# Performance work log

Hardware: AMD Instinct MI355X
Metric: run time of the kernel (lower is better)

The kernel has to match this reference:

```python
import jax, jax.numpy as jnp
import numpy as np

NUM_TOKENS = 2048
NUM_EXPERTS = 8
TOPK = 2
INTERMEDIATE = 2048
HIDDEN = 1024


def setup_inputs() -> dict:
    key = jax.random.key(0)
    k1, k2, k3 = jax.random.split(key, 3)
    intermediate_states = jax.random.normal(k1, (NUM_TOKENS * TOPK, INTERMEDIATE), dtype=jnp.float32)
    # per-expert down-projection, scaled like a typical init
    w = jax.random.normal(k2, (NUM_EXPERTS, INTERMEDIATE, HIDDEN), dtype=jnp.float32) / np.float32(np.sqrt(INTERMEDIATE))
    router_logits = jax.random.normal(k3, (NUM_TOKENS, NUM_EXPERTS), dtype=jnp.float32)
    return {"intermediate_states": intermediate_states, "w": w, "router_logits": router_logits}


def reference(intermediate_states, w, router_logits):
    T, E = router_logits.shape
    K = TOPK
    H = w.shape[-1]
    # Routing: softmax over experts, then top-k weights/ids (precompute_ctx.full_topk_weight/full_topk_ids)
    probs = jax.nn.softmax(router_logits, axis=-1)          # [T, E]
    topk_w, topk_ids = jax.lax.top_k(probs, K)              # [T, K]
    # Grouped expert GEMM: each (token, k) row is multiplied by its expert's weight.
    # Compute against all experts once, then gather the routed expert per row.
    out_all = jnp.einsum('ri,eih->reh', intermediate_states, w)   # [T*K, E, H]
    flat_ids = topk_ids.reshape(-1)                               # [T*K]
    routed = jnp.take_along_axis(out_all, flat_ids[:, None, None], axis=1)[:, 0, :]  # [T*K, H]
    # topk-weighted reduction over the K expert outputs per token
    out = (routed.reshape(T, K, H) * topk_w[..., None]).sum(axis=1)  # [T, H]
    # reduce-scatter across tensor-parallel ranks: with world_size=1 this is identity
    return out
```

## Files before the change

### kernel.cpp

```cpp
#include <hip/hip_runtime.h>

#define T_TOKENS 2048
#define N_EXPERTS 8
#define ROWS (T_TOKENS * 2)
#define I_DIM 2048
#define H_DIM 1024

#define M_TILE 128
#define N_TILE 128
#define BK 64
#define KSPLIT 2
#define KCHUNK (I_DIM / KSPLIT)
#define NSTEP (KCHUNK / BK)

typedef __bf16 bf16x8 __attribute__((ext_vector_type(8)));
typedef float f32x4 __attribute__((ext_vector_type(4)));

__device__ inline void load_lds16(const void* g, void* l) {
    __builtin_amdgcn_global_load_lds(
        (const __attribute__((address_space(1))) void*)g,
        (__attribute__((address_space(3))) void*)l, 16, 0, 0);
}

__global__ __launch_bounds__(256) void prep_kernel(
    const float* __restrict__ w, const float* __restrict__ x,
    const float* __restrict__ logits,
    __bf16* __restrict__ wT, __bf16* __restrict__ xB,
    float* __restrict__ out, float* __restrict__ topk_w,
    int* __restrict__ cnt, int* __restrict__ rowlist) {
    const int b = blockIdx.x;
    const int t = threadIdx.x;
    if (b < 2048) {
        __shared__ float tile[128 * 65];
        const int e = b >> 8;
        const int k0 = ((b >> 4) & 15) * 128;
        const int n0 = (b & 15) * 64;
        const float* ws = w + (size_t)e * (I_DIM * H_DIM) + (size_t)k0 * H_DIM + n0;
#pragma unroll
        for (int i = 0; i < 8; ++i) {
            int flat = i * 256 + t;
            int k = flat >> 4, nq = (flat & 15) * 4;
            f32x4 v = *(const f32x4*)(ws + (size_t)k * H_DIM + nq);
            float* d = &tile[k * 65 + nq];
            d[0] = v.x; d[1] = v.y; d[2] = v.z; d[3] = v.w;
        }
        __syncthreads();
        __bf16* wd = wT + (size_t)e * (H_DIM * I_DIM) + (size_t)n0 * I_DIM + k0;
#pragma unroll
        for (int j = 0; j < 4; ++j) {
            int flat = j * 256 + t;
            int n = flat >> 4, kc = (flat & 15) * 8;
            bf16x8 o;
#pragma unroll
            for (int q = 0; q < 8; ++q) o[q] = (__bf16)tile[(kc + q) * 65 + n];
            *(bf16x8*)(wd + (size_t)n * I_DIM + kc) = o;
        }
    } else if (b < 4096) {
        size_t base = ((size_t)(b - 2048) * 256 + t) * 16;
        const f32x4* xs = (const f32x4*)(x + base);
        f32x4 v0 = xs[0], v1 = xs[1], v2 = xs[2], v3 = xs[3];
        bf16x8 o0 = { (__bf16)v0.x, (__bf16)v0.y, (__bf16)v0.z, (__bf16)v0.w,
                      (__bf16)v1.x, (__bf16)v1.y, (__bf16)v1.z, (__bf16)v1.w };
        bf16x8 o1 = { (__bf16)v2.x, (__bf16)v2.y, (__bf16)v2.z, (__bf16)v2.w,
                      (__bf16)v3.x, (__bf16)v3.y, (__bf16)v3.z, (__bf16)v3.w };
        *(bf16x8*)(xB + base) = o0;
        *(bf16x8*)(xB + base + 8) = o1;
    } else if (b < 5120) {
        size_t idx = (size_t)(b - 4096) * 256 + t;
        f32x4 z = (f32x4){0.f, 0.f, 0.f, 0.f};
        ((f32x4*)out)[2 * idx] = z;
        ((f32x4*)out)[2 * idx + 1] = z;
    } else {
        __shared__ int lcnt[N_EXPERTS];
        if (t < N_EXPERTS) lcnt[t] = 0;
        __syncthreads();
#pragma unroll
        for (int i = 0; i < 8; ++i) {
            int tok = i * 256 + t;
            float l[8];
#pragma unroll
            for (int e = 0; e < 8; ++e) l[e] = logits[tok * 8 + e];
            float mx = l[0];
#pragma unroll
            for (int e = 1; e < 8; ++e) mx = fmaxf(mx, l[e]);
            float s = 0.f;
#pragma unroll
            for (int e = 0; e < 8; ++e) { l[e] = expf(l[e] - mx); s += l[e]; }
            float inv = 1.f / s;
            float v0 = -1.f, v1 = -1.f; int i0 = 0, i1 = 0;
#pragma unroll
            for (int e = 0; e < 8; ++e) {
                float p = l[e] * inv;
                if (p > v0)      { v1 = v0; i1 = i0; v0 = p; i0 = e; }
                else if (p > v1) { v1 = p; i1 = e; }
            }
            topk_w[2 * tok]     = v0;
            topk_w[2 * tok + 1] = v1;
            int p0 = atomicAdd(&lcnt[i0], 1); rowlist[i0 * ROWS + p0] = 2 * tok;
            int p1 = atomicAdd(&lcnt[i1], 1); rowlist[i1 * ROWS + p1] = 2 * tok + 1;
        }
        __syncthreads();
        if (t < N_EXPERTS) cnt[t] = lcnt[t];
    }
}

__global__ __launch_bounds__(256, 2) void gemm_kernel(
    const __bf16* __restrict__ xB, const __bf16* __restrict__ wT,
    const int* __restrict__ cnt, const int* __restrict__ rowlist,
    const float* __restrict__ topk_w, float* __restrict__ out) {
    const int e = blockIdx.y;
    const int cnt_e = cnt[e];
    const int m0 = blockIdx.z * M_TILE;
    if (m0 >= cnt_e) return;
    const int ntile = blockIdx.x & 7;
    const int khalf = blockIdx.x >> 3;
    const int n0 = ntile * N_TILE;
    const int tid = threadIdx.x;
    const int lane = tid & 63;
    const int wave = tid >> 6;
    const int wm = wave & 1, wn = wave >> 1;

    __shared__ __bf16 As[2][M_TILE * BK];
    __shared__ __bf16 Bs[2][N_TILE * BK];

    const int* rl = rowlist + e * ROWS;

    const int lc = lane & 7;
    const int lr = lane >> 3;
    const int cg = lc ^ lr;

    const __bf16* asrc[4];
#pragma unroll
    for (int i = 0; i < 4; ++i) {
        int gm = m0 + 32 * wave + 8 * i + lr;
        if (gm >= cnt_e) gm = cnt_e - 1;
        asrc[i] = xB + (size_t)rl[gm] * I_DIM + khalf * KCHUNK + cg * 8;
    }
    const __bf16* wTe = wT + (size_t)e * (H_DIM * I_DIM);
    const __bf16* bsrc = wTe + (size_t)(n0 + 32 * wave + lr) * I_DIM
                             + khalf * KCHUNK + cg * 8;

    const int lm = lane & 15, lg = lane >> 4, sw = lm & 7;
    int offA[2][4], offB[2][4];
#pragma unroll
    for (int s = 0; s < 2; ++s) {
        int cs = (((s * 4) + lg) ^ sw) * 8;
#pragma unroll
        for (int f = 0; f < 4; ++f) {
            offA[s][f] = (wm * 64 + f * 16 + lm) * BK + cs;
            offB[s][f] = (wn * 64 + f * 16 + lm) * BK + cs;
        }
    }

    f32x4 acc[4][4];
#pragma unroll
    for (int mt = 0; mt < 4; ++mt)
#pragma unroll
        for (int nt = 0; nt < 4; ++nt)
            acc[mt][nt] = (f32x4){0.f, 0.f, 0.f, 0.f};

#pragma unroll
    for (int i = 0; i < 4; ++i) {
        load_lds16(asrc[i], &As[0][(32 * wave + 8 * i) * BK]);
        load_lds16(bsrc + (size_t)(8 * i) * I_DIM, &Bs[0][(32 * wave + 8 * i) * BK]);
    }
    __syncthreads();

    for (int tstep = 0; tstep < NSTEP; ++tstep) {
        const int cur = tstep & 1;
        if (tstep + 1 < NSTEP) {
            const int koff = (tstep + 1) * BK;
#pragma unroll
            for (int i = 0; i < 4; ++i) {
                load_lds16(asrc[i] + koff, &As[cur ^ 1][(32 * wave + 8 * i) * BK]);
                load_lds16(bsrc + (size_t)(8 * i) * I_DIM + koff,
                           &Bs[cur ^ 1][(32 * wave + 8 * i) * BK]);
            }
        }
        const __bf16* Ab = As[cur];
        const __bf16* Bb = Bs[cur];
#pragma unroll
        for (int s = 0; s < 2; ++s) {
            bf16x8 af[4], bfr[4];
#pragma unroll
            for (int f = 0; f < 4; ++f) af[f] = *(const bf16x8*)&Ab[offA[s][f]];
#pragma unroll
            for (int f = 0; f < 4; ++f) bfr[f] = *(const bf16x8*)&Bb[offB[s][f]];
#pragma unroll
            for (int mt = 0; mt < 4; ++mt)
#pragma unroll
                for (int nt = 0; nt < 4; ++nt)
                    acc[mt][nt] = __builtin_amdgcn_mfma_f32_16x16x32_bf16(
                        af[mt], bfr[nt], acc[mt][nt], 0, 0, 0);
        }
        __syncthreads();
    }

    const int lq = lane >> 4, ln = lane & 15;
#pragma unroll
    for (int mt = 0; mt < 4; ++mt) {
#pragma unroll
        for (int j = 0; j < 4; ++j) {
            int gm = m0 + wm * 64 + mt * 16 + lq * 4 + j;
            if (gm < cnt_e) {
                int row = rl[gm];
                float tw = topk_w[row];
                float* orow = out + (size_t)(row >> 1) * H_DIM + n0 + wn * 64 + ln;
#pragma unroll
                for (int nt = 0; nt < 4; ++nt)
                    atomicAdd(&orow[nt * 16], acc[mt][nt][j] * tw);
            }
        }
    }
}

extern "C" void kernel_launch(void* const* d_in, const int* in_sizes, int n_in,
                              void* d_out, int out_size, void* d_ws, size_t ws_size,
                              hipStream_t stream) {
    const float* x      = (const float*)d_in[0];
    const float* w      = (const float*)d_in[1];
    const float* logits = (const float*)d_in[2];
    float* out = (float*)d_out;

    char* ws = (char*)d_ws;
    float*  topk_w  = (float*)ws;
    int*    cnt     = (int*)(ws + 16384);
    int*    rowlist = (int*)(ws + 16384 + 128);
    __bf16* wT      = (__bf16*)(ws + 16384 + 128 + 131072);
    __bf16* xB      = (__bf16*)(ws + 16384 + 128 + 131072 + 33554432);

    prep_kernel<<<5121, 256, 0, stream>>>(w, x, logits, wT, xB, out, topk_w, cnt, rowlist);
    gemm_kernel<<<dim3((H_DIM / N_TILE) * KSPLIT, N_EXPERTS, ROWS / M_TILE), 256, 0, stream>>>(
        xB, wT, cnt, rowlist, topk_w, out);
}
```

Before: 199.2 us.

## Drop split-K, shrink M tile to 64, and pipeline LDS loads with vmcnt waits

Removes the 2-way K split, so each GEMM block covers the full K dimension, and halves the M tile to 64 rows, which keeps a similar block count with fewer atomic adds to the output. The double-buffered global-to-LDS loads now wait on explicit vmcnt counts with raw s_barrier calls instead of __syncthreads, so the next stage's loads stay in flight during compute. Launch bounds move to 3 blocks per CU, and the routing block is moved to block 0 of the prep kernel so it is scheduled early. The cost is a K loop twice as long per block and less reuse of each B tile per M row.

Result: faster. 167.6 us (-15.8%).

```diff
diff --git a/kernel.cpp b/kernel.cpp
--- a/kernel.cpp
+++ b/kernel.cpp
@@ -6,12 +6,10 @@
 #define I_DIM 2048
 #define H_DIM 1024
 
-#define M_TILE 128
+#define M_TILE 64
 #define N_TILE 128
 #define BK 64
-#define KSPLIT 2
-#define KCHUNK (I_DIM / KSPLIT)
-#define NSTEP (KCHUNK / BK)
+#define NSTEP (I_DIM / BK)
 
 typedef __bf16 bf16x8 __attribute__((ext_vector_type(8)));
 typedef float f32x4 __attribute__((ext_vector_type(4)));
@@ -30,47 +28,7 @@
     int* __restrict__ cnt, int* __restrict__ rowlist) {
     const int b = blockIdx.x;
     const int t = threadIdx.x;
-    if (b < 2048) {
-        __shared__ float tile[128 * 65];
-        const int e = b >> 8;
-        const int k0 = ((b >> 4) & 15) * 128;
-        const int n0 = (b & 15) * 64;
-        const float* ws = w + (size_t)e * (I_DIM * H_DIM) + (size_t)k0 * H_DIM + n0;
-#pragma unroll
-        for (int i = 0; i < 8; ++i) {
-            int flat = i * 256 + t;
-            int k = flat >> 4, nq = (flat & 15) * 4;
-            f32x4 v = *(const f32x4*)(ws + (size_t)k * H_DIM + nq);
-            float* d = &tile[k * 65 + nq];
-            d[0] = v.x; d[1] = v.y; d[2] = v.z; d[3] = v.w;
-        }
-        __syncthreads();
-        __bf16* wd = wT + (size_t)e * (H_DIM * I_DIM) + (size_t)n0 * I_DIM + k0;
-#pragma unroll
-        for (int j = 0; j < 4; ++j) {
-            int flat = j * 256 + t;
-            int n = flat >> 4, kc = (flat & 15) * 8;
-            bf16x8 o;
-#pragma unroll
-            for (int q = 0; q < 8; ++q) o[q] = (__bf16)tile[(kc + q) * 65 + n];
-            *(bf16x8*)(wd + (size_t)n * I_DIM + kc) = o;
-        }
-    } else if (b < 4096) {
-        size_t base = ((size_t)(b - 2048) * 256 + t) * 16;
-        const f32x4* xs = (const f32x4*)(x + base);
-        f32x4 v0 = xs[0], v1 = xs[1], v2 = xs[2], v3 = xs[3];
-        bf16x8 o0 = { (__bf16)v0.x, (__bf16)v0.y, (__bf16)v0.z, (__bf16)v0.w,
-                      (__bf16)v1.x, (__bf16)v1.y, (__bf16)v1.z, (__bf16)v1.w };
-        bf16x8 o1 = { (__bf16)v2.x, (__bf16)v2.y, (__bf16)v2.z, (__bf16)v2.w,
-                      (__bf16)v3.x, (__bf16)v3.y, (__bf16)v3.z, (__bf16)v3.w };
-        *(bf16x8*)(xB + base) = o0;
-        *(bf16x8*)(xB + base + 8) = o1;
-    } else if (b < 5120) {
-        size_t idx = (size_t)(b - 4096) * 256 + t;
-        f32x4 z = (f32x4){0.f, 0.f, 0.f, 0.f};
-        ((f32x4*)out)[2 * idx] = z;
-        ((f32x4*)out)[2 * idx + 1] = z;
-    } else {
+    if (b == 0) {
         __shared__ int lcnt[N_EXPERTS];
         if (t < N_EXPERTS) lcnt[t] = 0;
         __syncthreads();
@@ -101,10 +59,51 @@
         }
         __syncthreads();
         if (t < N_EXPERTS) cnt[t] = lcnt[t];
-    }
-}
-
-__global__ __launch_bounds__(256, 2) void gemm_kernel(
+    } else if (b < 2049) {
+        const int bb = b - 1;
+        __shared__ float tile[128 * 65];
+        const int e = bb >> 8;
+        const int k0 = ((bb >> 4) & 15) * 128;
+        const int n0 = (bb & 15) * 64;
+        const float* ws = w + (size_t)e * (I_DIM * H_DIM) + (size_t)k0 * H_DIM + n0;
+#pragma unroll
+        for (int i = 0; i < 8; ++i) {
+            int flat = i * 256 + t;
+            int k = flat >> 4, nq = (flat & 15) * 4;
+            f32x4 v = *(const f32x4*)(ws + (size_t)k * H_DIM + nq);
+            float* d = &tile[k * 65 + nq];
+            d[0] = v.x; d[1] = v.y; d[2] = v.z; d[3] = v.w;
+        }
+        __syncthreads();
+        __bf16* wd = wT + (size_t)e * (H_DIM * I_DIM) + (size_t)n0 * I_DIM + k0;
+#pragma unroll
+        for (int j = 0; j < 4; ++j) {
+            int flat = j * 256 + t;
+            int n = flat >> 4, kc = (flat & 15) * 8;
+            bf16x8 o;
+#pragma unroll
+            for (int q = 0; q < 8; ++q) o[q] = (__bf16)tile[(kc + q) * 65 + n];
+            *(bf16x8*)(wd + (size_t)n * I_DIM + kc) = o;
+        }
+    } else if (b < 4097) {
+        size_t base = ((size_t)(b - 2049) * 256 + t) * 16;
+        const f32x4* xs = (const f32x4*)(x + base);
+        f32x4 v0 = xs[0], v1 = xs[1], v2 = xs[2], v3 = xs[3];
+        bf16x8 o0 = { (__bf16)v0.x, (__bf16)v0.y, (__bf16)v0.z, (__bf16)v0.w,
+                      (__bf16)v1.x, (__bf16)v1.y, (__bf16)v1.z, (__bf16)v1.w };
+        bf16x8 o1 = { (__bf16)v2.x, (__bf16)v2.y, (__bf16)v2.z, (__bf16)v2.w,
+                      (__bf16)v3.x, (__bf16)v3.y, (__bf16)v3.z, (__bf16)v3.w };
+        *(bf16x8*)(xB + base) = o0;
+        *(bf16x8*)(xB + base + 8) = o1;
+    } else {
+        size_t idx = (size_t)(b - 4097) * 256 + t;
+        f32x4 z = (f32x4){0.f, 0.f, 0.f, 0.f};
+        ((f32x4*)out)[2 * idx] = z;
+        ((f32x4*)out)[2 * idx + 1] = z;
+    }
+}
+
+__global__ __launch_bounds__(256, 3) void gemm_kernel(
     const __bf16* __restrict__ xB, const __bf16* __restrict__ wT,
     const int* __restrict__ cnt, const int* __restrict__ rowlist,
     const float* __restrict__ topk_w, float* __restrict__ out) {
@@ -112,9 +111,7 @@
     const int cnt_e = cnt[e];
     const int m0 = blockIdx.z * M_TILE;
     if (m0 >= cnt_e) return;
-    const int ntile = blockIdx.x & 7;
-    const int khalf = blockIdx.x >> 3;
-    const int n0 = ntile * N_TILE;
+    const int n0 = blockIdx.x * N_TILE;
     const int tid = threadIdx.x;
     const int lane = tid & 63;
     const int wave = tid >> 6;
@@ -129,79 +126,85 @@
     const int lr = lane >> 3;
     const int cg = lc ^ lr;
 
-    const __bf16* asrc[4];
-#pragma unroll
-    for (int i = 0; i < 4; ++i) {
-        int gm = m0 + 32 * wave + 8 * i + lr;
-        if (gm >= cnt_e) gm = cnt_e - 1;
-        asrc[i] = xB + (size_t)rl[gm] * I_DIM + khalf * KCHUNK + cg * 8;
-    }
+    int gm0 = m0 + 16 * wave + lr;
+    int gm1 = gm0 + 8;
+    if (gm0 >= cnt_e) gm0 = cnt_e - 1;
+    if (gm1 >= cnt_e) gm1 = cnt_e - 1;
+    const __bf16* asrc0 = xB + (size_t)rl[gm0] * I_DIM + cg * 8;
+    const __bf16* asrc1 = xB + (size_t)rl[gm1] * I_DIM + cg * 8;
     const __bf16* wTe = wT + (size_t)e * (H_DIM * I_DIM);
-    const __bf16* bsrc = wTe + (size_t)(n0 + 32 * wave + lr) * I_DIM
-                             + khalf * KCHUNK + cg * 8;
+    const __bf16* bsrc = wTe + (size_t)(n0 + 32 * wave + lr) * I_DIM + cg * 8;
 
     const int lm = lane & 15, lg = lane >> 4, sw = lm & 7;
-    int offA[2][4], offB[2][4];
+    int offA[2][2], offB[2][4];
 #pragma unroll
     for (int s = 0; s < 2; ++s) {
         int cs = (((s * 4) + lg) ^ sw) * 8;
 #pragma unroll
-        for (int f = 0; f < 4; ++f) {
-            offA[s][f] = (wm * 64 + f * 16 + lm) * BK + cs;
-            offB[s][f] = (wn * 64 + f * 16 + lm) * BK + cs;
-        }
-    }
-
-    f32x4 acc[4][4];
-#pragma unroll
-    for (int mt = 0; mt < 4; ++mt)
+        for (int mt = 0; mt < 2; ++mt)
+            offA[s][mt] = (wm * 32 + mt * 16 + lm) * BK + cs;
+#pragma unroll
+        for (int nt = 0; nt < 4; ++nt)
+            offB[s][nt] = (wn * 64 + nt * 16 + lm) * BK + cs;
+    }
+
+    f32x4 acc[2][4];
+#pragma unroll
+    for (int mt = 0; mt < 2; ++mt)
 #pragma unroll
         for (int nt = 0; nt < 4; ++nt)
             acc[mt][nt] = (f32x4){0.f, 0.f, 0.f, 0.f};
 
-#pragma unroll
-    for (int i = 0; i < 4; ++i) {
-        load_lds16(asrc[i], &As[0][(32 * wave + 8 * i) * BK]);
-        load_lds16(bsrc + (size_t)(8 * i) * I_DIM, &Bs[0][(32 * wave + 8 * i) * BK]);
-    }
-    __syncthreads();
-
-    for (int tstep = 0; tstep < NSTEP; ++tstep) {
-        const int cur = tstep & 1;
-        if (tstep + 1 < NSTEP) {
-            const int koff = (tstep + 1) * BK;
-#pragma unroll
-            for (int i = 0; i < 4; ++i) {
-                load_lds16(asrc[i] + koff, &As[cur ^ 1][(32 * wave + 8 * i) * BK]);
-                load_lds16(bsrc + (size_t)(8 * i) * I_DIM + koff,
-                           &Bs[cur ^ 1][(32 * wave + 8 * i) * BK]);
-            }
-        }
+#define STAGE(buf, koff)                                                  \
+    do {                                                                  \
+        load_lds16(asrc0 + (koff), &As[buf][wave * 1024]);                \
+        load_lds16(asrc1 + (koff), &As[buf][wave * 1024 + 512]);          \
+        load_lds16(bsrc + (koff),               &Bs[buf][wave * 2048]);   \
+        load_lds16(bsrc +  8 * I_DIM + (koff),  &Bs[buf][wave * 2048 + 512]);  \
+        load_lds16(bsrc + 16 * I_DIM + (koff),  &Bs[buf][wave * 2048 + 1024]); \
+        load_lds16(bsrc + 24 * I_DIM + (koff),  &Bs[buf][wave * 2048 + 1536]); \
+    } while (0)
+
+    STAGE(0, 0);
+
+    for (int t = 0; t < NSTEP; ++t) {
+        const int cur = t & 1;
+        if (t + 1 < NSTEP) {
+            STAGE(cur ^ 1, (t + 1) * BK);
+            asm volatile("s_waitcnt vmcnt(6)" ::: "memory");
+        } else {
+            asm volatile("s_waitcnt vmcnt(0)" ::: "memory");
+        }
+        __builtin_amdgcn_s_barrier();
+        asm volatile("" ::: "memory");
+
         const __bf16* Ab = As[cur];
         const __bf16* Bb = Bs[cur];
 #pragma unroll
         for (int s = 0; s < 2; ++s) {
-            bf16x8 af[4], bfr[4];
-#pragma unroll
-            for (int f = 0; f < 4; ++f) af[f] = *(const bf16x8*)&Ab[offA[s][f]];
+            bf16x8 af[2], bfr[4];
+#pragma unroll
+            for (int f = 0; f < 2; ++f) af[f] = *(const bf16x8*)&Ab[offA[s][f]];
 #pragma unroll
             for (int f = 0; f < 4; ++f) bfr[f] = *(const bf16x8*)&Bb[offB[s][f]];
 #pragma unroll
-            for (int mt = 0; mt < 4; ++mt)
+            for (int mt = 0; mt < 2; ++mt)
 #pragma unroll
                 for (int nt = 0; nt < 4; ++nt)
                     acc[mt][nt] = __builtin_amdgcn_mfma_f32_16x16x32_bf16(
                         af[mt], bfr[nt], acc[mt][nt], 0, 0, 0);
         }
-        __syncthreads();
-    }
+        asm volatile("" ::: "memory");
+        __builtin_amdgcn_s_barrier();
+    }
+#undef STAGE
 
     const int lq = lane >> 4, ln = lane & 15;
 #pragma unroll
-    for (int mt = 0; mt < 4; ++mt) {
+    for (int mt = 0; mt < 2; ++mt) {
 #pragma unroll
         for (int j = 0; j < 4; ++j) {
-            int gm = m0 + wm * 64 + mt * 16 + lq * 4 + j;
+            int gm = m0 + wm * 32 + mt * 16 + lq * 4 + j;
             if (gm < cnt_e) {
                 int row = rl[gm];
                 float tw = topk_w[row];
@@ -230,6 +233,6 @@
     __bf16* xB      = (__bf16*)(ws + 16384 + 128 + 131072 + 33554432);
 
     prep_kernel<<<5121, 256, 0, stream>>>(w, x, logits, wT, xB, out, topk_w, cnt, rowlist);
-    gemm_kernel<<<dim3((H_DIM / N_TILE) * KSPLIT, N_EXPERTS, ROWS / M_TILE), 256, 0, stream>>>(
+    gemm_kernel<<<dim3(H_DIM / N_TILE, N_EXPERTS, ROWS / M_TILE), 256, 0, stream>>>(
         xB, wT, cnt, rowlist, topk_w, out);
 }
```
